# Kernel optimization log

Hardware: AMD Instinct MI355X
Metric: run time of the kernel (lower is better)

## Reference

```python
import jax, jax.numpy as jnp
import numpy as np

N_HEADS = 64
HEAD_DIM = 128
ROPE_DIM = 64
INDEX_TOPK = 1024
LN_EPS = 1e-6


def hadamard_matrix(n):
    # Sylvester construction, scaled by n**-0.5 (matches fast_hadamard_transform scale)
    H = np.array([[1.0]])
    while H.shape[0] < n:
        H = np.block([[H, H], [H, -H]])
    return jnp.asarray(H * (n ** -0.5), dtype=jnp.float32)


def apply_rope_interleaved(x, cos, sin):
    # x: [B, S, H, rope_dim] with interleaved (real, imag) pairs; cos/sin: [S, rope_dim//2]
    xr, xi = x[..., 0::2], x[..., 1::2]
    c = cos[None, :, None, :]
    s = sin[None, :, None, :]
    yr = xr * c - xi * s
    yi = xr * s + xi * c
    return jnp.stack([yr, yi], axis=-1).reshape(x.shape)


def layernorm(x, w, b):
    mu = jnp.mean(x, axis=-1, keepdims=True)
    var = jnp.mean(jnp.square(x - mu), axis=-1, keepdims=True)
    return (x - mu) * jax.lax.rsqrt(var + LN_EPS) * w + b


def setup_inputs() -> dict:
    key = jax.random.key(0)
    ks = jax.random.split(key, 6)
    B, S, D, R = 1, 2048, 7168, 1536
    # proper rotary frequencies (rope_theta=10000)
    inv_freq = 1.0 / (10000.0 ** (np.arange(0, ROPE_DIM, 2, dtype=np.float32) / ROPE_DIM))
    ang = np.arange(S, dtype=np.float32)[:, None] * inv_freq[None, :]  # [S, 32]
    return {
        "hidden_states": jax.random.normal(ks[0], (B, S, D), jnp.float32),
        "q_lora": jax.random.normal(ks[1], (B, S, R), jnp.float32),
        "cos": jnp.asarray(np.cos(ang)),
        "sin": jnp.asarray(np.sin(ang)),
        "wq_b": jax.random.normal(ks[2], (R, N_HEADS * HEAD_DIM), jnp.float32) * (R ** -0.5),
        "wk_w": jax.random.normal(ks[3], (D, HEAD_DIM), jnp.float32) * (D ** -0.5),
        "k_norm_w": jnp.ones((HEAD_DIM,), jnp.float32),
        "k_norm_b": jnp.zeros((HEAD_DIM,), jnp.float32),
        "weights_proj_w": jax.random.normal(ks[4], (D, N_HEADS), jnp.float32) * (D ** -0.5),
    }


def reference(hidden_states, q_lora, cos, sin, wq_b, wk_w, k_norm_w, k_norm_b, weights_proj_w):
    B, S, _ = hidden_states.shape
    # indexer queries from q-LoRA latent
    q = (q_lora @ wq_b).reshape(B, S, N_HEADS, HEAD_DIM)
    q_pe = apply_rope_interleaved(q[..., :ROPE_DIM], cos, sin)
    q = jnp.concatenate([q_pe, q[..., ROPE_DIM:]], axis=-1)
    # single shared indexer key per token
    k = layernorm(hidden_states @ wk_w, k_norm_w, k_norm_b)  # [B, S, HEAD_DIM]
    k_pe = apply_rope_interleaved(k[..., :ROPE_DIM][:, :, None, :], cos, sin)[:, :, 0]
    k = jnp.concatenate([k_pe, k[..., ROPE_DIM:]], axis=-1)
    # Hadamard transform on q and k (scale = HEAD_DIM**-0.5)
    Hm = hadamard_matrix(HEAD_DIM)
    q = q @ Hm
    k = k @ Hm
    # per-head query weights
    w = (hidden_states @ weights_proj_w) * (N_HEADS ** -0.5)  # [B, S, N_HEADS]
    softmax_scale = HEAD_DIM ** -0.5
    # ReLU-weighted dot-product score over all key positions
    s_h = jnp.einsum("bshd,btd->bhst", q, k)  # [B, H, S, S]
    scores = jnp.einsum("bhst,bsh->bst", jax.nn.relu(s_h) * softmax_scale, w)
    causal = jnp.tril(jnp.ones((S, S), bool))
    scores = jnp.where(causal[None], scores, -jnp.inf)
    topk_idx = jax.lax.top_k(scores, INDEX_TOPK)[1]
    return scores, topk_idx
```

## Files before the change

### kernel.cpp

```cpp
#include <hip/hip_runtime.h>
#include <hip/hip_bf16.h>
#include <cstdint>
#include <cstddef>

#define S_LEN 2048
#define D_HID 7168
#define R_LORA 1536
#define NH 64
#define HD 128
#define QCOLS 8192
#define TOPK 1024
#define KW_CHUNKS 8
#define KW_KLEN (D_HID / KW_CHUNKS)
#define MASK_VAL (-1.0e30f)

typedef unsigned short u16;
typedef __attribute__((ext_vector_type(8))) short bf16x8;
typedef __attribute__((ext_vector_type(4))) float f32x4;

#define GLOAD16(g, l)                                                        \
  __builtin_amdgcn_global_load_lds(                                          \
      (const __attribute__((address_space(1))) void*)(g),                    \
      (__attribute__((address_space(3))) void*)(l), 16, 0, 0)

static __device__ __forceinline__ float4 ld4(const float* p) {
  return *reinterpret_cast<const float4*>(p);
}

static __device__ __forceinline__ f32x4 mfma16(bf16x8 a, bf16x8 b, f32x4 c) {
  return __builtin_amdgcn_mfma_f32_16x16x32_bf16(a, b, c, 0, 0, 0);
}

static __device__ __forceinline__ void split_bf16(float x, u16& hi, u16& lo) {
  __hip_bfloat16 h = __float2bfloat16(x);
  float hf = __bfloat162float(h);
  __hip_bfloat16 l = __float2bfloat16(x - hf);
  hi = *reinterpret_cast<u16*>(&h);
  lo = *reinterpret_cast<u16*>(&l);
}

__global__ __launch_bounds__(256) void cvt_split_kernel(
    const float* __restrict__ src, u16* __restrict__ dhi,
    u16* __restrict__ dlo) {
  const int i = (blockIdx.x * 256 + threadIdx.x) * 4;
  const float4 v = ld4(src + i);
  ushort4 h, l;
  split_bf16(v.x, h.x, l.x);
  split_bf16(v.y, h.y, l.y);
  split_bf16(v.z, h.z, l.z);
  split_bf16(v.w, h.w, l.w);
  *reinterpret_cast<ushort4*>(dhi + i) = h;
  *reinterpret_cast<ushort4*>(dlo + i) = l;
}

__global__ __launch_bounds__(256) void wkp_transpose_kernel(
    const float* __restrict__ wk, const float* __restrict__ wp,
    u16* __restrict__ wkthi, u16* __restrict__ wktlo) {
  __shared__ u16 th[64][72];
  __shared__ u16 tl[64][72];
  const int tid = threadIdx.x;
  const int k0 = blockIdx.x * 64;
  const int nb = blockIdx.y;

  const int r = tid >> 2;
  const int cq = tid & 3;
#pragma unroll
  for (int j = 0; j < 4; ++j) {
    const int c = cq * 16 + j * 4;
    float4 v;
    if (nb < 2) v = ld4(&wk[(size_t)(k0 + r) * HD + nb * 64 + c]);
    else        v = ld4(&wp[(size_t)(k0 + r) * NH + c]);
    u16 h, l;
    split_bf16(v.x, h, l); th[r][c + 0] = h; tl[r][c + 0] = l;
    split_bf16(v.y, h, l); th[r][c + 1] = h; tl[r][c + 1] = l;
    split_bf16(v.z, h, l); th[r][c + 2] = h; tl[r][c + 2] = l;
    split_bf16(v.w, h, l); th[r][c + 3] = h; tl[r][c + 3] = l;
  }
  __syncthreads();

  const int nl = tid >> 2;
  const int kc = tid & 3;
  u16 oh[16], ol[16];
#pragma unroll
  for (int j = 0; j < 16; ++j) {
    oh[j] = th[kc * 16 + j][nl];
    ol[j] = tl[kc * 16 + j][nl];
  }
  const size_t o = (size_t)(nb * 64 + nl) * D_HID + k0 + kc * 16;
  *reinterpret_cast<bf16x8*>(wkthi + o) = *reinterpret_cast<bf16x8*>(&oh[0]);
  *reinterpret_cast<bf16x8*>(wkthi + o + 8) = *reinterpret_cast<bf16x8*>(&oh[8]);
  *reinterpret_cast<bf16x8*>(wktlo + o) = *reinterpret_cast<bf16x8*>(&ol[0]);
  *reinterpret_cast<bf16x8*>(wktlo + o + 8) = *reinterpret_cast<bf16x8*>(&ol[8]);
}

__global__ __launch_bounds__(256) void kw_mfma_kernel(
    const u16* __restrict__ hhi, const u16* __restrict__ hlo,
    const u16* __restrict__ wkthi, const u16* __restrict__ wktlo,
    float* __restrict__ part) {
  __shared__ u16 lds[32768];
  const int tid = threadIdx.x;
  const int m_blk = blockIdx.x * 64;
  const int k_beg = blockIdx.y * KW_KLEN;

  const int lane = tid & 63;
  const int wv = tid >> 6;
  const int lr = lane & 15, lq = lane >> 4;
  const int wave_n = wv * 48;

  const int a_row = wv * 16 + (lane >> 2);
  const int a_clog = (lane & 3) ^ ((a_row >> 1) & 3);
  const u16* sAh = hhi + (size_t)(m_blk + a_row) * D_HID + k_beg + a_clog * 8;
  const u16* sAl = hlo + (size_t)(m_blk + a_row) * D_HID + k_beg + a_clog * 8;
  u16* dAh = lds + wv * 512;
  u16* dAl = lds + 2048 + wv * 512;

  const u16* sBh[3]; const u16* sBl[3];
  u16* dBh[3]; u16* dBl[3];
#pragma unroll
  for (int i = 0; i < 3; ++i) {
    const int j = wv * 3 + i;
    const int b_row = j * 16 + (lane >> 2);
    const int b_clog = (lane & 3) ^ ((b_row >> 1) & 3);
    sBh[i] = wkthi + (size_t)b_row * D_HID + k_beg + b_clog * 8;
    sBl[i] = wktlo + (size_t)b_row * D_HID + k_beg + b_clog * 8;
    dBh[i] = lds + 4096 + j * 512;
    dBl[i] = lds + 10240 + j * 512;
  }

  int aoff[4], boff[3];
#pragma unroll
  for (int mf = 0; mf < 4; ++mf) {
    const int row = mf * 16 + lr;
    aoff[mf] = row * 32 + (lq ^ ((row >> 1) & 3)) * 8;
  }
#pragma unroll
  for (int nf = 0; nf < 3; ++nf) {
    const int row = wave_n + nf * 16 + lr;
    boff[nf] = row * 32 + (lq ^ ((row >> 1) & 3)) * 8;
  }

  f32x4 acc[4][3];
#pragma unroll
  for (int a = 0; a < 4; ++a)
#pragma unroll
    for (int b = 0; b < 3; ++b) acc[a][b] = (f32x4){0.f, 0.f, 0.f, 0.f};

  auto STAGE = [&](int buf) {
    const int nb = buf * 16384;
    GLOAD16(sAh, dAh + nb);
    GLOAD16(sAl, dAl + nb);
#pragma unroll
    for (int i = 0; i < 3; ++i) {
      GLOAD16(sBh[i], dBh[i] + nb);
      GLOAD16(sBl[i], dBl[i] + nb);
      sBh[i] += 32; sBl[i] += 32;
    }
    sAh += 32; sAl += 32;
  };

  const int NT = KW_KLEN / 32;
  STAGE(0);
  asm volatile("s_waitcnt vmcnt(0)" ::: "memory");
  __syncthreads();

  for (int ks = 0; ks < NT; ++ks) {
    if (ks + 1 < NT) STAGE((ks + 1) & 1);

    const u16* base = lds + (ks & 1) * 16384;
    bf16x8 ah[4], al[4], bh[3], bl[3];
#pragma unroll
    for (int mf = 0; mf < 4; ++mf) {
      ah[mf] = *reinterpret_cast<const bf16x8*>(base + aoff[mf]);
      al[mf] = *reinterpret_cast<const bf16x8*>(base + 2048 + aoff[mf]);
    }
#pragma unroll
    for (int nf = 0; nf < 3; ++nf) {
      bh[nf] = *reinterpret_cast<const bf16x8*>(base + 4096 + boff[nf]);
      bl[nf] = *reinterpret_cast<const bf16x8*>(base + 10240 + boff[nf]);
    }
#pragma unroll
    for (int mf = 0; mf < 4; ++mf)
#pragma unroll
      for (int nf = 0; nf < 3; ++nf) {
        acc[mf][nf] = mfma16(ah[mf], bh[nf], acc[mf][nf]);
        acc[mf][nf] = mfma16(ah[mf], bl[nf], acc[mf][nf]);
        acc[mf][nf] = mfma16(al[mf], bh[nf], acc[mf][nf]);
      }

    asm volatile("s_waitcnt vmcnt(0)" ::: "memory");
    __syncthreads();
  }

  float* pbase = part + (size_t)blockIdx.y * S_LEN * 192;
#pragma unroll
  for (int mf = 0; mf < 4; ++mf) {
    const int sG = m_blk + mf * 16 + lq * 4;
#pragma unroll
    for (int nf = 0; nf < 3; ++nf) {
      const int col = wave_n + nf * 16 + lr;
      float* p = pbase + (size_t)sG * 192 + col;
#pragma unroll
      for (int i = 0; i < 4; ++i) p[(size_t)i * 192] = acc[mf][nf][i];
    }
  }
}

__global__ __launch_bounds__(256) void w_reduce_kernel(
    const float* __restrict__ part, float* __restrict__ w_red) {
  const int i = blockIdx.x * 256 + threadIdx.x;
  if (i >= S_LEN * NH) return;
  const int s = i >> 6, h = i & 63;
  float v = 0.f;
#pragma unroll
  for (int c = 0; c < KW_CHUNKS; ++c)
    v += part[((size_t)c * S_LEN + s) * 192 + 128 + h];
  w_red[i] = v;
}

__global__ __launch_bounds__(64) void k_finalize_kernel(
    const float* __restrict__ part, const float* __restrict__ cosb,
    const float* __restrict__ sinb, const float* __restrict__ knw,
    const float* __restrict__ knb, u16* __restrict__ khi,
    u16* __restrict__ klo) {
  const int s = blockIdx.x;
  const int lane = threadIdx.x;
  float x0 = 0.f, x1 = 0.f;
#pragma unroll
  for (int c = 0; c < KW_CHUNKS; ++c) {
    const float* p = part + ((size_t)c * S_LEN + s) * 192;
    x0 += p[lane];
    x1 += p[lane + 64];
  }
  float red = x0 + x1;
#pragma unroll
  for (int off = 32; off >= 1; off >>= 1) red += __shfl_xor(red, off);
  const float mu = red * (1.f / 128.f);
  const float d0 = x0 - mu, d1 = x1 - mu;
  float v = d0 * d0 + d1 * d1;
#pragma unroll
  for (int off = 32; off >= 1; off >>= 1) v += __shfl_xor(v, off);
  const float inv = rsqrtf(v * (1.f / 128.f) + 1e-6f);
  const float y0 = d0 * inv * knw[lane] + knb[lane];
  const float y1 = d1 * inv * knw[lane + 64] + knb[lane + 64];
  const float partner = __shfl_xor(y0, 1);
  const int i = lane >> 1;
  const float c = cosb[s * 32 + i], sn = sinb[s * 32 + i];
  float r;
  if ((lane & 1) == 0) r = y0 * c - partner * sn;
  else                 r = partner * sn + y0 * c;
  u16 h0, l0, h1, l1;
  split_bf16(r, h0, l0);
  split_bf16(y1, h1, l1);
  khi[(size_t)s * HD + lane] = h0;
  klo[(size_t)s * HD + lane] = l0;
  khi[(size_t)s * HD + 64 + lane] = h1;
  klo[(size_t)s * HD + 64 + lane] = l1;
}

__global__ __launch_bounds__(256) void wqb_transpose_kernel(
    const float* __restrict__ wqb, u16* __restrict__ wthi,
    u16* __restrict__ wtlo) {
  __shared__ u16 th[64][72];
  __shared__ u16 tl[64][72];
  const int tid = threadIdx.x;
  const int n0 = blockIdx.x * 64;
  const int k0 = blockIdx.y * 64;

  const int r = tid >> 2;
  const int cq = tid & 3;
#pragma unroll
  for (int j = 0; j < 4; ++j) {
    const int c = cq * 16 + j * 4;
    const float4 v = ld4(&wqb[(size_t)(k0 + r) * QCOLS + n0 + c]);
    u16 h, l;
    split_bf16(v.x, h, l); th[r][c + 0] = h; tl[r][c + 0] = l;
    split_bf16(v.y, h, l); th[r][c + 1] = h; tl[r][c + 1] = l;
    split_bf16(v.z, h, l); th[r][c + 2] = h; tl[r][c + 2] = l;
    split_bf16(v.w, h, l); th[r][c + 3] = h; tl[r][c + 3] = l;
  }
  __syncthreads();

  const int nl = tid >> 2;
  const int kc = tid & 3;
  u16 oh[16], ol[16];
#pragma unroll
  for (int j = 0; j < 16; ++j) {
    oh[j] = th[kc * 16 + j][nl];
    ol[j] = tl[kc * 16 + j][nl];
  }
  const size_t o = (size_t)(n0 + nl) * R_LORA + k0 + kc * 16;
  *reinterpret_cast<bf16x8*>(wthi + o) = *reinterpret_cast<bf16x8*>(&oh[0]);
  *reinterpret_cast<bf16x8*>(wthi + o + 8) = *reinterpret_cast<bf16x8*>(&oh[8]);
  *reinterpret_cast<bf16x8*>(wtlo + o) = *reinterpret_cast<bf16x8*>(&ol[0]);
  *reinterpret_cast<bf16x8*>(wtlo + o + 8) = *reinterpret_cast<bf16x8*>(&ol[8]);
}

__global__ __launch_bounds__(512) void q_gemm_mfma_kernel(
    const u16* __restrict__ qlhi, const u16* __restrict__ qllo,
    const u16* __restrict__ wthi, const u16* __restrict__ wtlo,
    const float* __restrict__ cosb, const float* __restrict__ sinb,
    u16* __restrict__ qhi, u16* __restrict__ qlo) {
  __shared__ u16 lds[65536];
  const int tid = threadIdx.x;
  const int bid = blockIdx.x;
  const int xcd = bid & 7, pos = bid >> 3;
  const int n_blk = (xcd * 4 + (pos & 3)) * 256;
  const int m_blk = (pos >> 2) * 256;

  const u16* srcA_hi[2]; const u16* srcA_lo[2];
  const u16* srcB_hi[2]; const u16* srcB_lo[2];
  int slot8[2];
#pragma unroll
  for (int i = 0; i < 2; ++i) {
    const int slot = tid + i * 512;
    const int row = slot >> 2;
    const int clog = (slot & 3) ^ ((row >> 1) & 3);
    slot8[i] = slot * 8;
    srcA_hi[i] = wthi + (size_t)(n_blk + row) * R_LORA + clog * 8;
    srcA_lo[i] = wtlo + (size_t)(n_blk + row) * R_LORA + clog * 8;
    srcB_hi[i] = qlhi + (size_t)(m_blk + row) * R_LORA + clog * 8;
    srcB_lo[i] = qllo + (size_t)(m_blk + row) * R_LORA + clog * 8;
  }

  const int wv = tid >> 6, lane = tid & 63;
  const int lr = lane & 15, lq = lane >> 4;
  const int wave_n = (wv & 3) * 64;
  const int wave_m = (wv >> 2) * 128;

  f32x4 acc[4][8];
#pragma unroll
  for (int a = 0; a < 4; ++a)
#pragma unroll
    for (int b = 0; b < 8; ++b) acc[a][b] = (f32x4){0.f, 0.f, 0.f, 0.f};

  int aoff[4], boff[8];
#pragma unroll
  for (int a = 0; a < 4; ++a) {
    const int rn = wave_n + a * 16 + lr;
    aoff[a] = rn * 32 + (lq ^ ((rn >> 1) & 3)) * 8;
  }
#pragma unroll
  for (int b = 0; b < 8; ++b) {
    const int rm = wave_m + b * 16 + lr;
    boff[b] = rm * 32 + (lq ^ ((rm >> 1) & 3)) * 8;
  }

  auto STAGE = [&](int buf) {
    u16* base = lds + buf * 32768;
#pragma unroll
    for (int i = 0; i < 2; ++i) {
      GLOAD16(srcA_hi[i], base + slot8[i]);
      GLOAD16(srcA_lo[i], base + 8192 + slot8[i]);
      GLOAD16(srcB_hi[i], base + 16384 + slot8[i]);
      GLOAD16(srcB_lo[i], base + 24576 + slot8[i]);
      srcA_hi[i] += 32; srcA_lo[i] += 32;
      srcB_hi[i] += 32; srcB_lo[i] += 32;
    }
  };

  const int NT = R_LORA / 32;
  STAGE(0);
  asm volatile("s_waitcnt vmcnt(0)" ::: "memory");
  __syncthreads();

  for (int t = 0; t < NT; ++t) {
    if (t + 1 < NT) STAGE((t + 1) & 1);

    const u16* base = lds + (t & 1) * 32768;
    bf16x8 ah[4], al[4];
#pragma unroll
    for (int a = 0; a < 4; ++a) {
      ah[a] = *reinterpret_cast<const bf16x8*>(base + aoff[a]);
      al[a] = *reinterpret_cast<const bf16x8*>(base + 8192 + aoff[a]);
    }
#pragma unroll
    for (int b = 0; b < 8; ++b) {
      const bf16x8 bh = *reinterpret_cast<const bf16x8*>(base + 16384 + boff[b]);
      const bf16x8 bl = *reinterpret_cast<const bf16x8*>(base + 24576 + boff[b]);
#pragma unroll
      for (int a = 0; a < 4; ++a) {
        acc[a][b] = mfma16(ah[a], bh, acc[a][b]);
        acc[a][b] = mfma16(ah[a], bl, acc[a][b]);
        acc[a][b] = mfma16(al[a], bh, acc[a][b]);
      }
    }

    asm volatile("s_waitcnt vmcnt(0)" ::: "memory");
    __syncthreads();
  }

#pragma unroll
  for (int a = 0; a < 4; ++a) {
    const int n_base = n_blk + wave_n + a * 16 + lq * 4;
    const bool rope = ((n_base & 127) < 64);
    const int i0 = (n_base & 63) >> 1;
#pragma unroll
    for (int b = 0; b < 8; ++b) {
      const int sG = m_blk + wave_m + b * 16 + lr;
      float4 v = make_float4(acc[a][b][0], acc[a][b][1], acc[a][b][2],
                             acc[a][b][3]);
      if (rope) {
        const float c0 = cosb[sG * 32 + i0], s0_ = sinb[sG * 32 + i0];
        const float c1 = cosb[sG * 32 + i0 + 1], s1_ = sinb[sG * 32 + i0 + 1];
        const float xr0 = v.x, xi0 = v.y, xr1 = v.z, xi1 = v.w;
        v.x = xr0 * c0 - xi0 * s0_;
        v.y = xr0 * s0_ + xi0 * c0;
        v.z = xr1 * c1 - xi1 * s1_;
        v.w = xr1 * s1_ + xi1 * c1;
      }
      ushort4 vh, vl;
      split_bf16(v.x, vh.x, vl.x);
      split_bf16(v.y, vh.y, vl.y);
      split_bf16(v.z, vh.z, vl.z);
      split_bf16(v.w, vh.w, vl.w);
      const size_t o = (size_t)sG * QCOLS + n_base;
      *reinterpret_cast<ushort4*>(qhi + o) = vh;
      *reinterpret_cast<ushort4*>(qlo + o) = vl;
    }
  }
}

__global__ __launch_bounds__(256, 2) void scores_mfma_kernel(
    const u16* __restrict__ qhi, const u16* __restrict__ qlo,
    const u16* __restrict__ khi, const u16* __restrict__ klo,
    const float* __restrict__ w_red, float* __restrict__ scores) {
  const int bid = blockIdx.x;
  const int xcd = bid & 7, pos = bid >> 3;
  const int jj = pos >> 5, xx = pos & 31;
  const int yy = (jj < 2) ? (2 * xcd + jj) : (31 - 2 * xcd - (3 - jj));
  const int t0 = xx * 64;
  const int s0 = yy * 64;
  const int tid = threadIdx.x;

  if (t0 > s0 + 63) {
    const int tx = tid & 15, ty = tid >> 4;
    const float4 mv = make_float4(MASK_VAL, MASK_VAL, MASK_VAL, MASK_VAL);
#pragma unroll
    for (int i = 0; i < 4; ++i) {
      const int sG = s0 + (ty << 2) + i;
      *reinterpret_cast<float4*>(&scores[(size_t)sG * S_LEN + t0 + (tx << 2)]) = mv;
    }
    return;
  }

  __shared__ u16 ldsQ[32768];
  __shared__ float ldsW[4096];

  const int lane = tid & 63;
  const int wv_id = tid >> 6;
  const int lr = lane & 15;
  const int lq = lane >> 4;

  bf16x8 Bh[4][4], Bl[4][4];
#pragma unroll
  for (int nf = 0; nf < 4; ++nf) {
    const int t = t0 + nf * 16 + lr;
#pragma unroll
    for (int ks = 0; ks < 4; ++ks) {
      const size_t off = (size_t)t * HD + ks * 32 + lq * 8;
      Bh[nf][ks] = *reinterpret_cast<const bf16x8*>(khi + off);
      Bl[nf][ks] = *reinterpret_cast<const bf16x8*>(klo + off);
    }
  }

#pragma unroll
  for (int jw = 0; jw < 16; ++jw) {
    const int idx = jw * 256 + tid;
    const int row = idx >> 6, h = idx & 63;
    ldsW[h * 64 + row] = w_red[(size_t)(s0 + row) * NH + h];
  }

  f32x4 tot[4];
#pragma unroll
  for (int nf = 0; nf < 4; ++nf) tot[nf] = (f32x4){0.f, 0.f, 0.f, 0.f};

  const int srow = tid >> 4;
  const int scb = (tid & 15) ^ (srow & 7);

  auto STAGE = [&](int h, int buf) {
    const size_t gb =
        (size_t)(s0 + srow) * QCOLS + (size_t)h * HD + scb * 8;
    u16* ldst = ldsQ + buf * 16384 + tid * 8;
#pragma unroll
    for (int j2 = 0; j2 < 4; ++j2) {
      GLOAD16(qhi + gb + (size_t)(16 * j2) * QCOLS, ldst + j2 * 2048);
      GLOAD16(qlo + gb + (size_t)(16 * j2) * QCOLS, ldst + 8192 + j2 * 2048);
    }
  };

  STAGE(0, 0);
  STAGE(1, 1);

  const int arow = wv_id * 16 + lr;
  const int sbl = wv_id * 16 + lq * 4;
  const int s_base = s0 + sbl;

  for (int h = 0; h < NH; ++h) {
    if (h < NH - 1) asm volatile("s_waitcnt vmcnt(8)" ::: "memory");
    else            asm volatile("s_waitcnt vmcnt(0)" ::: "memory");
    __syncthreads();

    const u16* base = ldsQ + (h & 1) * 16384;
    const float4 wv4 =
        *reinterpret_cast<const float4*>(&ldsW[h * 64 + sbl]);

    f32x4 acc[4];
#pragma unroll
    for (int nf = 0; nf < 4; ++nf) acc[nf] = (f32x4){0.f, 0.f, 0.f, 0.f};

#pragma unroll
    for (int ks = 0; ks < 4; ++ks) {
      const int akb = ks * 4 + lq;
      const int abyte = arow * 128 + ((akb ^ (arow & 7)) * 8);
      const bf16x8 ah = *reinterpret_cast<const bf16x8*>(base + abyte);
      const bf16x8 al = *reinterpret_cast<const bf16x8*>(base + 8192 + abyte);
#pragma unroll
      for (int nf = 0; nf < 4; ++nf) {
        acc[nf] = mfma16(ah, Bh[nf][ks], acc[nf]);
        acc[nf] = mfma16(ah, Bl[nf][ks], acc[nf]);
        acc[nf] = mfma16(al, Bh[nf][ks], acc[nf]);
      }
    }

    const float wvv[4] = {wv4.x, wv4.y, wv4.z, wv4.w};
#pragma unroll
    for (int nf = 0; nf < 4; ++nf) {
#pragma unroll
      for (int i = 0; i < 4; ++i)
        tot[nf][i] += fmaxf(acc[nf][i], 0.f) * wvv[i];
    }

    __syncthreads();
    if (h + 2 < NH) STAGE(h + 2, h & 1);
  }

  const float cscale = 0.011048543456039806f;
#pragma unroll
  for (int nf = 0; nf < 4; ++nf) {
    const int tcol = t0 + nf * 16 + lr;
#pragma unroll
    for (int i = 0; i < 4; ++i) {
      const int sG = s_base + i;
      scores[(size_t)sG * S_LEN + tcol] =
          (tcol <= sG) ? cscale * tot[nf][i] : MASK_VAL;
    }
  }
}

__global__ __launch_bounds__(512) void topk_kernel(
    const float* __restrict__ scores, int* __restrict__ topk) {
  __shared__ unsigned long long keys[S_LEN];
  const int s = blockIdx.x;
  const int m = s + 1;
  int n2 = 1;
  while (n2 < m) n2 <<= 1;
  const int tid = threadIdx.x;

  for (int t = tid; t < n2; t += 512) {
    unsigned long long kk;
    if (t < m) {
      const unsigned int b = __float_as_uint(scores[(size_t)s * S_LEN + t]);
      const unsigned int sb = b ^ ((unsigned int)((int)b >> 31) | 0x80000000u);
      kk = ((unsigned long long)(~sb) << 32) | (unsigned int)t;
    } else {
      kk = ~0ull;
    }
    keys[t] = kk;
  }
  __syncthreads();

  for (int k = 2; k <= n2; k <<= 1) {
    for (int j = k >> 1; j > 0; j >>= 1) {
      const int half = n2 >> 1;
      for (int p = tid; p < half; p += 512) {
        const int idx = ((p & ~(j - 1)) << 1) | (p & (j - 1));
        const int pa = idx | j;
        const bool up = ((idx & k) == 0);
        const unsigned long long a = keys[idx], b = keys[pa];
        if ((a > b) == up) { keys[idx] = b; keys[pa] = a; }
      }
      __syncthreads();
    }
  }

  for (int p = tid; p < TOPK; p += 512) {
    topk[(size_t)s * TOPK + p] = (p < m) ? (int)(keys[p] & 0xFFFFFFFFu) : p;
  }
}

extern "C" void kernel_launch(void* const* d_in, const int* in_sizes, int n_in,
                              void* d_out, int out_size, void* d_ws, size_t ws_size,
                              hipStream_t stream) {
  const float* hidden = (const float*)d_in[0];
  const float* q_lora = (const float*)d_in[1];
  const float* cosb   = (const float*)d_in[2];
  const float* sinb   = (const float*)d_in[3];
  const float* wq_b   = (const float*)d_in[4];
  const float* wk_w   = (const float*)d_in[5];
  const float* knw    = (const float*)d_in[6];
  const float* knb    = (const float*)d_in[7];
  const float* wproj  = (const float*)d_in[8];

  float* scores_out = (float*)d_out;
  int* topk_out = (int*)(scores_out + (size_t)S_LEN * S_LEN);

  char* ws = (char*)d_ws;
  u16* qhi    = (u16*)(ws + 0);
  u16* qlo    = (u16*)(ws + 33554432);
  u16* hhi    = (u16*)(ws + 0);
  u16* hlo    = (u16*)(ws + 33554432);
  u16* khi    = (u16*)(ws + 67108864);
  u16* klo    = (u16*)(ws + 67633152);
  float* w_ws = (float*)(ws + 68157440);
  u16* qlhi   = (u16*)(ws + 68681728);
  u16* qllo   = (u16*)(ws + 74973184);
  u16* wthi   = (u16*)(ws + 81264640);
  u16* wtlo   = (u16*)(ws + 106430464);
  u16* wkthi  = (u16*)(ws + 131596288);
  u16* wktlo  = (u16*)(ws + 134348800);
  float* part = (float*)(ws + 137101312);

  hipLaunchKernelGGL(cvt_split_kernel, dim3((S_LEN * D_HID) / 1024), dim3(256),
                     0, stream, hidden, hhi, hlo);
  hipLaunchKernelGGL(wkp_transpose_kernel, dim3(D_HID / 64, 3), dim3(256), 0,
                     stream, wk_w, wproj, wkthi, wktlo);
  hipLaunchKernelGGL(kw_mfma_kernel, dim3(S_LEN / 64, KW_CHUNKS), dim3(256), 0,
                     stream, hhi, hlo, wkthi, wktlo, part);
  hipLaunchKernelGGL(w_reduce_kernel, dim3((S_LEN * NH) / 256), dim3(256), 0,
                     stream, part, w_ws);
  hipLaunchKernelGGL(k_finalize_kernel, dim3(S_LEN), dim3(64), 0, stream,
                     part, cosb, sinb, knw, knb, khi, klo);
  hipLaunchKernelGGL(cvt_split_kernel, dim3((S_LEN * R_LORA) / 1024),
                     dim3(256), 0, stream, q_lora, qlhi, qllo);
  hipLaunchKernelGGL(wqb_transpose_kernel, dim3(QCOLS / 64, R_LORA / 64),
                     dim3(256), 0, stream, wq_b, wthi, wtlo);
  hipLaunchKernelGGL(q_gemm_mfma_kernel, dim3(256), dim3(512), 0, stream,
                     qlhi, qllo, wthi, wtlo, cosb, sinb, qhi, qlo);
  hipLaunchKernelGGL(scores_mfma_kernel, dim3(32 * 32), dim3(256), 0, stream,
                     qhi, qlo, khi, klo, w_ws, scores_out);
  hipLaunchKernelGGL(topk_kernel, dim3(S_LEN), dim3(512), 0, stream,
                     scores_out, topk_out);
}
```

Baseline: 422.7 us.

## Deepen LDS prefetch pipeline and issue next-stage loads before MFMA compute

The K/weights-projection GEMM goes from single-buffer-ahead staging to a two-deep prefetch, using combined waitcnt+barrier macros. In both that kernel and the scores kernel, LDS fragments are read into registers first, then a barrier is taken and the next global-to-LDS stage is issued before the MFMA block rather than after it. This lets memory loads overlap compute and drops one barrier per iteration. MFMA sections are wrapped in s_setprio to favour issuing matrix instructions, at the cost of more registers held for the preloaded fragments.

```diff
diff --git a/kernel.cpp b/kernel.cpp
--- a/kernel.cpp
+++ b/kernel.cpp
@@ -22,6 +22,10 @@
   __builtin_amdgcn_global_load_lds(                                          \
       (const __attribute__((address_space(1))) void*)(g),                    \
       (__attribute__((address_space(3))) void*)(l), 16, 0, 0)
+
+#define BAR_VM8()  asm volatile("s_waitcnt vmcnt(8)\n\ts_barrier" ::: "memory")
+#define BAR_VM0()  asm volatile("s_waitcnt vmcnt(0)\n\ts_barrier" ::: "memory")
+#define BAR_LGKM() asm volatile("s_waitcnt lgkmcnt(0)\n\ts_barrier" ::: "memory")
 
 static __device__ __forceinline__ float4 ld4(const float* p) {
   return *reinterpret_cast<const float4*>(p);
@@ -160,11 +164,11 @@
 
   const int NT = KW_KLEN / 32;
   STAGE(0);
-  asm volatile("s_waitcnt vmcnt(0)" ::: "memory");
-  __syncthreads();
+  STAGE(1);
 
   for (int ks = 0; ks < NT; ++ks) {
-    if (ks + 1 < NT) STAGE((ks + 1) & 1);
+    if (ks < NT - 1) BAR_VM8();
+    else             BAR_VM0();
 
     const u16* base = lds + (ks & 1) * 16384;
     bf16x8 ah[4], al[4], bh[3], bl[3];
@@ -178,6 +182,10 @@
       bh[nf] = *reinterpret_cast<const bf16x8*>(base + 4096 + boff[nf]);
       bl[nf] = *reinterpret_cast<const bf16x8*>(base + 10240 + boff[nf]);
     }
+    BAR_LGKM();
+    if (ks + 2 < NT) STAGE(ks & 1);
+
+    __builtin_amdgcn_s_setprio(1);
 #pragma unroll
     for (int mf = 0; mf < 4; ++mf)
 #pragma unroll
@@ -186,9 +194,7 @@
         acc[mf][nf] = mfma16(ah[mf], bl[nf], acc[mf][nf]);
         acc[mf][nf] = mfma16(al[mf], bh[nf], acc[mf][nf]);
       }
-
-    asm volatile("s_waitcnt vmcnt(0)" ::: "memory");
-    __syncthreads();
+    __builtin_amdgcn_s_setprio(0);
   }
 
   float* pbase = part + (size_t)blockIdx.y * S_LEN * 192;
@@ -490,37 +496,46 @@
 
   STAGE(0, 0);
   STAGE(1, 1);
+  BAR_LGKM();
 
   const int arow = wv_id * 16 + lr;
   const int sbl = wv_id * 16 + lq * 4;
   const int s_base = s0 + sbl;
 
   for (int h = 0; h < NH; ++h) {
-    if (h < NH - 1) asm volatile("s_waitcnt vmcnt(8)" ::: "memory");
-    else            asm volatile("s_waitcnt vmcnt(0)" ::: "memory");
-    __syncthreads();
+    if (h < NH - 1) BAR_VM8();
+    else            BAR_VM0();
 
     const u16* base = ldsQ + (h & 1) * 16384;
     const float4 wv4 =
         *reinterpret_cast<const float4*>(&ldsW[h * 64 + sbl]);
 
-    f32x4 acc[4];
-#pragma unroll
-    for (int nf = 0; nf < 4; ++nf) acc[nf] = (f32x4){0.f, 0.f, 0.f, 0.f};
-
+    bf16x8 ah[4], al[4];
 #pragma unroll
     for (int ks = 0; ks < 4; ++ks) {
       const int akb = ks * 4 + lq;
       const int abyte = arow * 128 + ((akb ^ (arow & 7)) * 8);
-      const bf16x8 ah = *reinterpret_cast<const bf16x8*>(base + abyte);
-      const bf16x8 al = *reinterpret_cast<const bf16x8*>(base + 8192 + abyte);
+      ah[ks] = *reinterpret_cast<const bf16x8*>(base + abyte);
+      al[ks] = *reinterpret_cast<const bf16x8*>(base + 8192 + abyte);
+    }
+    BAR_LGKM();
+    if (h + 2 < NH) STAGE(h + 2, h & 1);
+
+    f32x4 acc[4];
+#pragma unroll
+    for (int nf = 0; nf < 4; ++nf) acc[nf] = (f32x4){0.f, 0.f, 0.f, 0.f};
+
+    __builtin_amdgcn_s_setprio(1);
+#pragma unroll
+    for (int ks = 0; ks < 4; ++ks) {
 #pragma unroll
       for (int nf = 0; nf < 4; ++nf) {
-        acc[nf] = mfma16(ah, Bh[nf][ks], acc[nf]);
-        acc[nf] = mfma16(ah, Bl[nf][ks], acc[nf]);
-        acc[nf] = mfma16(al, Bh[nf][ks], acc[nf]);
+        acc[nf] = mfma16(ah[ks], Bh[nf][ks], acc[nf]);
+        acc[nf] = mfma16(ah[ks], Bl[nf][ks], acc[nf]);
+        acc[nf] = mfma16(al[ks], Bh[nf][ks], acc[nf]);
       }
     }
+    __builtin_amdgcn_s_setprio(0);
 
     const float wvv[4] = {wv4.x, wv4.y, wv4.z, wv4.w};
 #pragma unroll
@@ -529,9 +544,6 @@
       for (int i = 0; i < 4; ++i)
         tot[nf][i] += fmaxf(acc[nf][i], 0.f) * wvv[i];
     }
-
-    __syncthreads();
-    if (h + 2 < NH) STAGE(h + 2, h & 1);
   }
 
   const float cscale = 0.011048543456039806f;
```

Result: slower. 439.1 us (+3.9%).

## Retile scores kernel to 32-row tiles and double-buffer kw GEMM stages

Applied to the files above, without the earlier changes.

The scores kernel now uses 32x64 output tiles, with four waves split two by two over rows and columns. The launch grid doubles and launch bounds are raised to allow four blocks per CU. The finer tiles cut wasted work on diagonal causal tiles and raise occupancy to hide Q load latency, at the cost of loading each K tile twice as often. Separately, the kw GEMM now prefetches two stages ahead, uses explicit waitcnt/barrier pairs, and raises wave priority around the MFMA block so global-to-LDS loads overlap compute.

```diff
diff --git a/kernel.cpp b/kernel.cpp
--- a/kernel.cpp
+++ b/kernel.cpp
@@ -22,6 +22,10 @@
   __builtin_amdgcn_global_load_lds(                                          \
       (const __attribute__((address_space(1))) void*)(g),                    \
       (__attribute__((address_space(3))) void*)(l), 16, 0, 0)
+
+#define BAR_VM8()  asm volatile("s_waitcnt vmcnt(8)\n\ts_barrier" ::: "memory")
+#define BAR_VM0()  asm volatile("s_waitcnt vmcnt(0)\n\ts_barrier" ::: "memory")
+#define BAR_LGKM() asm volatile("s_waitcnt lgkmcnt(0)\n\ts_barrier" ::: "memory")
 
 static __device__ __forceinline__ float4 ld4(const float* p) {
   return *reinterpret_cast<const float4*>(p);
@@ -160,11 +164,11 @@
 
   const int NT = KW_KLEN / 32;
   STAGE(0);
-  asm volatile("s_waitcnt vmcnt(0)" ::: "memory");
-  __syncthreads();
+  STAGE(1);
 
   for (int ks = 0; ks < NT; ++ks) {
-    if (ks + 1 < NT) STAGE((ks + 1) & 1);
+    if (ks < NT - 1) BAR_VM8();
+    else             BAR_VM0();
 
     const u16* base = lds + (ks & 1) * 16384;
     bf16x8 ah[4], al[4], bh[3], bl[3];
@@ -178,6 +182,10 @@
       bh[nf] = *reinterpret_cast<const bf16x8*>(base + 4096 + boff[nf]);
       bl[nf] = *reinterpret_cast<const bf16x8*>(base + 10240 + boff[nf]);
     }
+    BAR_LGKM();
+    if (ks + 2 < NT) STAGE(ks & 1);
+
+    __builtin_amdgcn_s_setprio(1);
 #pragma unroll
     for (int mf = 0; mf < 4; ++mf)
 #pragma unroll
@@ -186,9 +194,7 @@
         acc[mf][nf] = mfma16(ah[mf], bl[nf], acc[mf][nf]);
         acc[mf][nf] = mfma16(al[mf], bh[nf], acc[mf][nf]);
       }
-
-    asm volatile("s_waitcnt vmcnt(0)" ::: "memory");
-    __syncthreads();
+    __builtin_amdgcn_s_setprio(0);
   }
 
   float* pbase = part + (size_t)blockIdx.y * S_LEN * 192;
@@ -420,41 +426,45 @@
   }
 }
 
-__global__ __launch_bounds__(256, 2) void scores_mfma_kernel(
+__global__ __launch_bounds__(256, 4) void scores_mfma_kernel(
     const u16* __restrict__ qhi, const u16* __restrict__ qlo,
     const u16* __restrict__ khi, const u16* __restrict__ klo,
     const float* __restrict__ w_red, float* __restrict__ scores) {
   const int bid = blockIdx.x;
   const int xcd = bid & 7, pos = bid >> 3;
-  const int jj = pos >> 5, xx = pos & 31;
-  const int yy = (jj < 2) ? (2 * xcd + jj) : (31 - 2 * xcd - (3 - jj));
+  const int jj = pos >> 5;
+  const int xx = pos & 31;
+  const int yy = (jj < 4) ? (xcd * 4 + jj) : (63 - (xcd * 4 + (jj - 4)));
   const int t0 = xx * 64;
-  const int s0 = yy * 64;
+  const int s0 = yy * 32;
   const int tid = threadIdx.x;
 
-  if (t0 > s0 + 63) {
-    const int tx = tid & 15, ty = tid >> 4;
+  if (t0 > s0 + 31) {
     const float4 mv = make_float4(MASK_VAL, MASK_VAL, MASK_VAL, MASK_VAL);
-#pragma unroll
-    for (int i = 0; i < 4; ++i) {
-      const int sG = s0 + (ty << 2) + i;
-      *reinterpret_cast<float4*>(&scores[(size_t)sG * S_LEN + t0 + (tx << 2)]) = mv;
+    const int r = tid >> 4;
+    const int c4 = (tid & 15) << 2;
+#pragma unroll
+    for (int i = 0; i < 2; ++i) {
+      const int sG = s0 + r + 16 * i;
+      *reinterpret_cast<float4*>(&scores[(size_t)sG * S_LEN + t0 + c4]) = mv;
     }
     return;
   }
 
-  __shared__ u16 ldsQ[32768];
-  __shared__ float ldsW[4096];
+  __shared__ u16 ldsQ[16384];
+  __shared__ float ldsW[2048];
 
   const int lane = tid & 63;
   const int wv_id = tid >> 6;
+  const int sv = wv_id >> 1;
+  const int tv = wv_id & 1;
   const int lr = lane & 15;
   const int lq = lane >> 4;
 
-  bf16x8 Bh[4][4], Bl[4][4];
-#pragma unroll
-  for (int nf = 0; nf < 4; ++nf) {
-    const int t = t0 + nf * 16 + lr;
+  bf16x8 Bh[2][4], Bl[2][4];
+#pragma unroll
+  for (int nf = 0; nf < 2; ++nf) {
+    const int t = t0 + tv * 32 + nf * 16 + lr;
 #pragma unroll
     for (int ks = 0; ks < 4; ++ks) {
       const size_t off = (size_t)t * HD + ks * 32 + lq * 8;
@@ -464,15 +474,15 @@
   }
 
 #pragma unroll
-  for (int jw = 0; jw < 16; ++jw) {
+  for (int jw = 0; jw < 8; ++jw) {
     const int idx = jw * 256 + tid;
     const int row = idx >> 6, h = idx & 63;
-    ldsW[h * 64 + row] = w_red[(size_t)(s0 + row) * NH + h];
-  }
-
-  f32x4 tot[4];
-#pragma unroll
-  for (int nf = 0; nf < 4; ++nf) tot[nf] = (f32x4){0.f, 0.f, 0.f, 0.f};
+    ldsW[h * 32 + row] = w_red[(size_t)(s0 + row) * NH + h];
+  }
+
+  f32x4 tot[2];
+#pragma unroll
+  for (int nf = 0; nf < 2; ++nf) tot[nf] = (f32x4){0.f, 0.f, 0.f, 0.f};
 
   const int srow = tid >> 4;
   const int scb = (tid & 15) ^ (srow & 7);
@@ -480,42 +490,39 @@
   auto STAGE = [&](int h, int buf) {
     const size_t gb =
         (size_t)(s0 + srow) * QCOLS + (size_t)h * HD + scb * 8;
-    u16* ldst = ldsQ + buf * 16384 + tid * 8;
-#pragma unroll
-    for (int j2 = 0; j2 < 4; ++j2) {
-      GLOAD16(qhi + gb + (size_t)(16 * j2) * QCOLS, ldst + j2 * 2048);
-      GLOAD16(qlo + gb + (size_t)(16 * j2) * QCOLS, ldst + 8192 + j2 * 2048);
-    }
+    u16* ldst = ldsQ + buf * 8192 + tid * 8;
+    GLOAD16(qhi + gb, ldst);
+    GLOAD16(qhi + gb + (size_t)16 * QCOLS, ldst + 2048);
+    GLOAD16(qlo + gb, ldst + 4096);
+    GLOAD16(qlo + gb + (size_t)16 * QCOLS, ldst + 6144);
   };
 
   STAGE(0, 0);
   STAGE(1, 1);
 
-  const int arow = wv_id * 16 + lr;
-  const int sbl = wv_id * 16 + lq * 4;
+  const int arow = sv * 16 + lr;
+  const int sbl = sv * 16 + lq * 4;
   const int s_base = s0 + sbl;
 
   for (int h = 0; h < NH; ++h) {
-    if (h < NH - 1) asm volatile("s_waitcnt vmcnt(8)" ::: "memory");
-    else            asm volatile("s_waitcnt vmcnt(0)" ::: "memory");
     __syncthreads();
 
-    const u16* base = ldsQ + (h & 1) * 16384;
+    const u16* base = ldsQ + (h & 1) * 8192;
     const float4 wv4 =
-        *reinterpret_cast<const float4*>(&ldsW[h * 64 + sbl]);
-
-    f32x4 acc[4];
-#pragma unroll
-    for (int nf = 0; nf < 4; ++nf) acc[nf] = (f32x4){0.f, 0.f, 0.f, 0.f};
+        *reinterpret_cast<const float4*>(&ldsW[h * 32 + sbl]);
+
+    f32x4 acc[2];
+#pragma unroll
+    for (int nf = 0; nf < 2; ++nf) acc[nf] = (f32x4){0.f, 0.f, 0.f, 0.f};
 
 #pragma unroll
     for (int ks = 0; ks < 4; ++ks) {
       const int akb = ks * 4 + lq;
       const int abyte = arow * 128 + ((akb ^ (arow & 7)) * 8);
       const bf16x8 ah = *reinterpret_cast<const bf16x8*>(base + abyte);
-      const bf16x8 al = *reinterpret_cast<const bf16x8*>(base + 8192 + abyte);
-#pragma unroll
-      for (int nf = 0; nf < 4; ++nf) {
+      const bf16x8 al = *reinterpret_cast<const bf16x8*>(base + 4096 + abyte);
+#pragma unroll
+      for (int nf = 0; nf < 2; ++nf) {
         acc[nf] = mfma16(ah, Bh[nf][ks], acc[nf]);
         acc[nf] = mfma16(ah, Bl[nf][ks], acc[nf]);
         acc[nf] = mfma16(al, Bh[nf][ks], acc[nf]);
@@ -524,7 +531,7 @@
 
     const float wvv[4] = {wv4.x, wv4.y, wv4.z, wv4.w};
 #pragma unroll
-    for (int nf = 0; nf < 4; ++nf) {
+    for (int nf = 0; nf < 2; ++nf) {
 #pragma unroll
       for (int i = 0; i < 4; ++i)
         tot[nf][i] += fmaxf(acc[nf][i], 0.f) * wvv[i];
@@ -536,8 +543,8 @@
 
   const float cscale = 0.011048543456039806f;
 #pragma unroll
-  for (int nf = 0; nf < 4; ++nf) {
-    const int tcol = t0 + nf * 16 + lr;
+  for (int nf = 0; nf < 2; ++nf) {
+    const int tcol = t0 + tv * 32 + nf * 16 + lr;
 #pragma unroll
     for (int i = 0; i < 4; ++i) {
       const int sG = s_base + i;
@@ -636,7 +643,7 @@
                      dim3(256), 0, stream, wq_b, wthi, wtlo);
   hipLaunchKernelGGL(q_gemm_mfma_kernel, dim3(256), dim3(512), 0, stream,
                      qlhi, qllo, wthi, wtlo, cosb, sinb, qhi, qlo);
-  hipLaunchKernelGGL(scores_mfma_kernel, dim3(32 * 32), dim3(256), 0, stream,
+  hipLaunchKernelGGL(scores_mfma_kernel, dim3(64 * 32), dim3(256), 0, stream,
                      qhi, qlo, khi, klo, w_ws, scores_out);
   hipLaunchKernelGGL(topk_kernel, dim3(S_LEN), dim3(512), 0, stream,
                      scores_out, topk_out);
```

Result: faster. 401.8 us (-5.0%).
